# Optimization experiments

Hardware: AMD Instinct MI355X
Metric: run time of the kernel (lower is better)

Reference implementation:

```python
import jax, jax.numpy as jnp
import numpy as np

B, CIN, H, W = 128, 64, 32, 32
COUT, K, STRIDE, PAD = 64, 3, 1, 1
HO = (H + 2 * PAD - K) // STRIDE + 1
WO = (W + 2 * PAD - K) // STRIDE + 1


def setup_inputs() -> dict:
    key = jax.random.key(0)
    k1, k2 = jax.random.split(key)
    x = jax.random.normal(k1, (B, CIN, H, W), dtype=jnp.float32)
    # weight scaled like torch init: randn / sqrt(k*k*Cin) (orthogonal_ in torch just
    # re-orthogonalizes; scale here matches the fan-in normalization)
    weight = jax.random.normal(k2, (HO, WO, COUT, CIN, K, K), dtype=jnp.float32) / np.sqrt(K * K * CIN)
    bias = jnp.full((COUT, HO, WO), 0.5, dtype=jnp.float32)
    return {"x": x, "weight": weight, "bias": bias}


def reference(x, weight, bias):
    # pad spatial dims
    xp = jnp.pad(x, ((0, 0), (0, 0), (PAD, PAD), (PAD, PAD)))
    # gather row windows: [B, C, Ho, K, Wp]
    ri = (jnp.arange(HO) * STRIDE)[:, None] + jnp.arange(K)[None, :]  # [Ho, K]
    ci = (jnp.arange(WO) * STRIDE)[:, None] + jnp.arange(K)[None, :]  # [Wo, K]
    rows = xp[:, :, ri, :]           # [B, C, Ho, K, Wp]
    patches = rows[:, :, :, :, ci]   # [B, C, Ho, K, Wo, K]
    # per-location matmul: b c h p w q , h w d c p q -> b d h w
    out = jnp.einsum('bchpwq,hwdcpq->bdhw', patches, weight)
    return out + bias[None]
```

## Files before the change

### kernel.cpp

```cpp
#include <hip/hip_runtime.h>
#include <hip/hip_bf16.h>

#define KT 576

typedef __attribute__((ext_vector_type(8))) short  short8;
typedef __attribute__((ext_vector_type(4))) float  f32x4;

__device__ __forceinline__ unsigned short f2bf(float f) {
  union { float f; unsigned int u; } v; v.f = f;
  return (unsigned short)((v.u + 0x7FFFu + ((v.u >> 16) & 1u)) >> 16);
}

__global__ __launch_bounds__(256) void xC2_kernel(const float* __restrict__ x,
                                                  unsigned short* __restrict__ xC2) {
  const int hp = blockIdx.x, bb = blockIdx.y, t = threadIdx.x;
  __shared__ unsigned short tile[32 * 1024];
  const bool interior = (hp >= 1 && hp <= 32);
  if (interior) {
#pragma unroll 4
    for (int i = 0; i < 32; ++i) {
      const int row = i * 32 + (t >> 3);
      const int bl = row >> 6, c = row & 63;
      const int k = t & 7;
      const float4 v = *(const float4*)(x + ((size_t)(bb * 16 + bl) * 64 + c) * 1024 +
                                        (hp - 1) * 32 + k * 4);
      const int base = (k * 4) * 1024 + (c >> 3) * 128 + bl * 8 + (c & 7);
      tile[base]        = f2bf(v.x);
      tile[base + 1024] = f2bf(v.y);
      tile[base + 2048] = f2bf(v.z);
      tile[base + 3072] = f2bf(v.w);
    }
  }
  __syncthreads();
  unsigned short* dst = xC2 + (size_t)hp * 278528 + (size_t)bb * 1024;
  const uint4 z = make_uint4(0u, 0u, 0u, 0u);
  for (int idx = t; idx < 34 * 128; idx += 256) {
    const int wp = idx >> 7, s = idx & 127;
    uint4 v = z;
    if (interior && wp >= 1 && wp <= 32) v = *(const uint4*)&tile[(wp - 1) * 1024 + s * 8];
    *(uint4*)(dst + (size_t)wp * 8192 + s * 8) = v;
  }
}

__global__ __launch_bounds__(256, 4) void lc_main(const float* __restrict__ Wt,
                                                  const float* __restrict__ bias,
                                                  const unsigned short* __restrict__ xC2,
                                                  float* __restrict__ out,
                                                  float* __restrict__ tmp,
                                                  int useTmp) {
  __shared__ unsigned short Wl[32 * KT];
  __shared__ float blds[32];

  const int bid = (int)blockIdx.x;
  const int swz = (bid & 7) * 256 + (bid >> 3);
  const int hw = swz >> 1, half = swz & 1;
  const int h = hw >> 5, w = hw & 31;
  const int t = threadIdx.x, lane = t & 63, wv = t >> 6;
  const int l15 = lane & 15, lg = lane >> 4;

  if (t < 32) blds[t] = bias[(half * 32 + t) * 1024 + hw];

  const float* Wsrc = Wt + (size_t)hw * (64 * KT) + (size_t)half * (32 * KT);
  float4 wreg[18];
#pragma unroll
  for (int i = 0; i < 18; ++i)
    wreg[i] = ((const float4*)Wsrc)[i * 256 + t];
#pragma unroll
  for (int i = 0; i < 18; ++i) {
    const int f = (i * 256 + t) * 4;
    const int d = (((unsigned)(f >> 6)) * 7282u) >> 16;
    int kn = f - d * 576;
    int c = ((unsigned)kn * 7282u) >> 16;
    int r = kn - c * 9;
    const float vv[4] = {wreg[i].x, wreg[i].y, wreg[i].z, wreg[i].w};
#pragma unroll
    for (int j = 0; j < 4; ++j) {
      const int kp = r * 64 + c;
      const int slot = (kp >> 3) ^ (d & 7);
      Wl[d * KT + slot * 8 + (kp & 7)] = f2bf(vv[j]);
      if (++r == 9) { r = 0; ++c; }
    }
  }
  __syncthreads();

  const unsigned short* xA = xC2 + (size_t)wv * 2048 + lg * 128 + l15 * 8;

  f32x4 acc[2][2];
#pragma unroll
  for (int bt = 0; bt < 2; ++bt)
#pragma unroll
    for (int dt = 0; dt < 2; ++dt) acc[bt][dt] = (f32x4){0.f, 0.f, 0.f, 0.f};

  const int x7 = l15 & 7;
  const int wrow0 = l15 * KT;
  const int wrow1 = (16 + l15) * KT;

  short8 A0[2][3], A1[2][3];
#pragma unroll
  for (int s = 0; s < 3; ++s) {
    const int pq = s >> 1, p = pq / 3, q = pq - p * 3;
    const size_t off = (size_t)(h + p) * 278528 + (size_t)(w + q) * 8192 + (s & 1) * 512;
    A0[0][s] = *(const short8*)(xA + off);
    A1[0][s] = *(const short8*)(xA + off + 1024);
  }
#pragma unroll
  for (int g = 0; g < 6; ++g) {
    const int cur = g & 1;
    if (g < 5) {
#pragma unroll
      for (int s = 0; s < 3; ++s) {
        const int step = (g + 1) * 3 + s;
        const int pq = step >> 1, p = pq / 3, q = pq - p * 3;
        const size_t off = (size_t)(h + p) * 278528 + (size_t)(w + q) * 8192 + (step & 1) * 512;
        A0[cur ^ 1][s] = *(const short8*)(xA + off);
        A1[cur ^ 1][s] = *(const short8*)(xA + off + 1024);
      }
    }
#pragma unroll
    for (int s = 0; s < 3; ++s) {
      const int step = g * 3 + s;
      const int sb = step * 4 + lg;
      const short8 b0 = *(const short8*)&Wl[wrow0 + ((sb ^ x7) << 3)];
      const short8 b1 = *(const short8*)&Wl[wrow1 + ((sb ^ x7) << 3)];
      acc[0][0] = __builtin_amdgcn_mfma_f32_16x16x32_bf16(A0[cur][s], b0, acc[0][0], 0, 0, 0);
      acc[1][0] = __builtin_amdgcn_mfma_f32_16x16x32_bf16(A1[cur][s], b0, acc[1][0], 0, 0, 0);
      acc[0][1] = __builtin_amdgcn_mfma_f32_16x16x32_bf16(A0[cur][s], b1, acc[0][1], 0, 0, 0);
      acc[1][1] = __builtin_amdgcn_mfma_f32_16x16x32_bf16(A1[cur][s], b1, acc[1][1], 0, 0, 0);
    }
  }

  if (useTmp) {
    float* tb = tmp + (size_t)(hw * 2 + half) * (32 * 128) + wv * 32;
#pragma unroll
    for (int dt = 0; dt < 2; ++dt) {
      const float bv = blds[dt * 16 + l15];
#pragma unroll
      for (int bt = 0; bt < 2; ++bt) {
        f32x4 v = acc[bt][dt];
        v[0] += bv; v[1] += bv; v[2] += bv; v[3] += bv;
        *(f32x4*)(tb + (dt * 16 + l15) * 128 + bt * 16 + lg * 4) = v;
      }
    }
  } else {
#pragma unroll
    for (int dt = 0; dt < 2; ++dt) {
      const int dg = half * 32 + dt * 16 + l15;
      const float bv = blds[dt * 16 + l15];
#pragma unroll
      for (int bt = 0; bt < 2; ++bt) {
#pragma unroll
        for (int i = 0; i < 4; ++i) {
          const int b = wv * 32 + bt * 16 + lg * 4 + i;
          out[(size_t)b * 65536 + (size_t)dg * 1024 + hw] = acc[bt][dt][i] + bv;
        }
      }
    }
  }
}

__global__ __launch_bounds__(256) void tr_out(const float* __restrict__ tmp,
                                              float* __restrict__ out) {
  const int h = blockIdx.x;
  const int d = blockIdx.y;
  const int half = d >> 5, dl = d & 31;
  const int t = threadIdx.x;
  __shared__ float ls[32 * 132];
  {
    const int w = t >> 3, bc = t & 7;
    const float* src = tmp + ((size_t)((h * 32 + w) * 2 + half) * 32 + dl) * 128 + bc * 16;
    float* dst = ls + w * 132 + bc * 16;
#pragma unroll
    for (int k = 0; k < 4; ++k) ((float4*)dst)[k] = ((const float4*)src)[k];
  }
  __syncthreads();
  {
    const int b = t >> 1, wh = t & 1;
    float4 o[4];
#pragma unroll
    for (int k = 0; k < 4; ++k)
#pragma unroll
      for (int j = 0; j < 4; ++j)
        ((float*)&o[k])[j] = ls[(wh * 16 + k * 4 + j) * 132 + b];
    float* dst = out + (size_t)b * 65536 + (size_t)d * 1024 + h * 32 + wh * 16;
#pragma unroll
    for (int k = 0; k < 4; ++k) ((float4*)dst)[k] = o[k];
  }
}

extern "C" void kernel_launch(void* const* d_in, const int* in_sizes, int n_in,
                              void* d_out, int out_size, void* d_ws, size_t ws_size,
                              hipStream_t stream) {
  const float* x    = (const float*)d_in[0];
  const float* wt   = (const float*)d_in[1];
  const float* bias = (const float*)d_in[2];
  float* out        = (float*)d_out;

  unsigned short* xC2 = (unsigned short*)d_ws;
  const size_t XC2_BYTES = 18939904u;
  const size_t TMP_BYTES = 33554432u;
  const int useTmp = (ws_size >= XC2_BYTES + TMP_BYTES) ? 1 : 0;
  float* tmp = (float*)((char*)d_ws + XC2_BYTES);

  xC2_kernel<<<dim3(34, 8), 256, 0, stream>>>(x, xC2);
  lc_main<<<2048, 256, 0, stream>>>(wt, bias, xC2, out, tmp, useTmp);
  if (useTmp) tr_out<<<dim3(32, 64), 256, 0, stream>>>(tmp, out);
}
```

Baseline: 72.85 us.

## Drop transposed temp buffer pass and write output directly; split weight loads into batches

Removes the intermediate tmp buffer and the separate transpose kernel, so the main kernel always scatters results straight to the output with strided 4-byte stores. The weight staging is split into two batches of nine float4 loads with a scheduling barrier, which lowers register pressure. The change saves a 32MB round trip through memory and one launch, but the direct stores are uncoalesced, one element per 4KB stride.

After: 83.05 us. 14.0% more time.

```diff
diff --git a/kernel.cpp b/kernel.cpp
--- a/kernel.cpp
+++ b/kernel.cpp
@@ -45,9 +45,7 @@
 __global__ __launch_bounds__(256, 4) void lc_main(const float* __restrict__ Wt,
                                                   const float* __restrict__ bias,
                                                   const unsigned short* __restrict__ xC2,
-                                                  float* __restrict__ out,
-                                                  float* __restrict__ tmp,
-                                                  int useTmp) {
+                                                  float* __restrict__ out) {
   __shared__ unsigned short Wl[32 * KT];
   __shared__ float blds[32];
 
@@ -61,24 +59,28 @@
   if (t < 32) blds[t] = bias[(half * 32 + t) * 1024 + hw];
 
   const float* Wsrc = Wt + (size_t)hw * (64 * KT) + (size_t)half * (32 * KT);
-  float4 wreg[18];
 #pragma unroll
-  for (int i = 0; i < 18; ++i)
-    wreg[i] = ((const float4*)Wsrc)[i * 256 + t];
+  for (int bat = 0; bat < 2; ++bat) {
+    float4 wreg[9];
 #pragma unroll
-  for (int i = 0; i < 18; ++i) {
-    const int f = (i * 256 + t) * 4;
-    const int d = (((unsigned)(f >> 6)) * 7282u) >> 16;
-    int kn = f - d * 576;
-    int c = ((unsigned)kn * 7282u) >> 16;
-    int r = kn - c * 9;
-    const float vv[4] = {wreg[i].x, wreg[i].y, wreg[i].z, wreg[i].w};
+    for (int i = 0; i < 9; ++i)
+      wreg[i] = ((const float4*)Wsrc)[(bat * 9 + i) * 256 + t];
+    __builtin_amdgcn_sched_barrier(0);
 #pragma unroll
-    for (int j = 0; j < 4; ++j) {
-      const int kp = r * 64 + c;
-      const int slot = (kp >> 3) ^ (d & 7);
-      Wl[d * KT + slot * 8 + (kp & 7)] = f2bf(vv[j]);
-      if (++r == 9) { r = 0; ++c; }
+    for (int i = 0; i < 9; ++i) {
+      const int f = ((bat * 9 + i) * 256 + t) * 4;
+      const int d = (((unsigned)(f >> 6)) * 7282u) >> 16;
+      int kn = f - d * 576;
+      int c = ((unsigned)kn * 7282u) >> 16;
+      int r = kn - c * 9;
+      const float vv[4] = {wreg[i].x, wreg[i].y, wreg[i].z, wreg[i].w};
+#pragma unroll
+      for (int j = 0; j < 4; ++j) {
+        const int kp = r * 64 + c;
+        const int slot = (kp >> 3) ^ (d & 7);
+        Wl[d * KT + slot * 8 + (kp & 7)] = f2bf(vv[j]);
+        if (++r == 9) { r = 0; ++c; }
+      }
     }
   }
   __syncthreads();
@@ -129,61 +131,18 @@
     }
   }
 
-  if (useTmp) {
-    float* tb = tmp + (size_t)(hw * 2 + half) * (32 * 128) + wv * 32;
 #pragma unroll
-    for (int dt = 0; dt < 2; ++dt) {
-      const float bv = blds[dt * 16 + l15];
+  for (int dt = 0; dt < 2; ++dt) {
+    const int dg = half * 32 + dt * 16 + l15;
+    const float bv = blds[dt * 16 + l15];
 #pragma unroll
-      for (int bt = 0; bt < 2; ++bt) {
-        f32x4 v = acc[bt][dt];
-        v[0] += bv; v[1] += bv; v[2] += bv; v[3] += bv;
-        *(f32x4*)(tb + (dt * 16 + l15) * 128 + bt * 16 + lg * 4) = v;
+    for (int bt = 0; bt < 2; ++bt) {
+#pragma unroll
+      for (int i = 0; i < 4; ++i) {
+        const int b = wv * 32 + bt * 16 + lg * 4 + i;
+        out[(size_t)b * 65536 + (size_t)dg * 1024 + hw] = acc[bt][dt][i] + bv;
       }
     }
-  } else {
-#pragma unroll
-    for (int dt = 0; dt < 2; ++dt) {
-      const int dg = half * 32 + dt * 16 + l15;
-      const float bv = blds[dt * 16 + l15];
-#pragma unroll
-      for (int bt = 0; bt < 2; ++bt) {
-#pragma unroll
-        for (int i = 0; i < 4; ++i) {
-          const int b = wv * 32 + bt * 16 + lg * 4 + i;
-          out[(size_t)b * 65536 + (size_t)dg * 1024 + hw] = acc[bt][dt][i] + bv;
-        }
-      }
-    }
-  }
-}
-
-__global__ __launch_bounds__(256) void tr_out(const float* __restrict__ tmp,
-                                              float* __restrict__ out) {
-  const int h = blockIdx.x;
-  const int d = blockIdx.y;
-  const int half = d >> 5, dl = d & 31;
-  const int t = threadIdx.x;
-  __shared__ float ls[32 * 132];
-  {
-    const int w = t >> 3, bc = t & 7;
-    const float* src = tmp + ((size_t)((h * 32 + w) * 2 + half) * 32 + dl) * 128 + bc * 16;
-    float* dst = ls + w * 132 + bc * 16;
-#pragma unroll
-    for (int k = 0; k < 4; ++k) ((float4*)dst)[k] = ((const float4*)src)[k];
-  }
-  __syncthreads();
-  {
-    const int b = t >> 1, wh = t & 1;
-    float4 o[4];
-#pragma unroll
-    for (int k = 0; k < 4; ++k)
-#pragma unroll
-      for (int j = 0; j < 4; ++j)
-        ((float*)&o[k])[j] = ls[(wh * 16 + k * 4 + j) * 132 + b];
-    float* dst = out + (size_t)b * 65536 + (size_t)d * 1024 + h * 32 + wh * 16;
-#pragma unroll
-    for (int k = 0; k < 4; ++k) ((float4*)dst)[k] = o[k];
   }
 }
 
@@ -194,14 +153,8 @@
   const float* wt   = (const float*)d_in[1];
   const float* bias = (const float*)d_in[2];
   float* out        = (float*)d_out;
-
   unsigned short* xC2 = (unsigned short*)d_ws;
-  const size_t XC2_BYTES = 18939904u;
-  const size_t TMP_BYTES = 33554432u;
-  const int useTmp = (ws_size >= XC2_BYTES + TMP_BYTES) ? 1 : 0;
-  float* tmp = (float*)((char*)d_ws + XC2_BYTES);
 
   xC2_kernel<<<dim3(34, 8), 256, 0, stream>>>(x, xC2);
-  lc_main<<<2048, 256, 0, stream>>>(wt, bias, xC2, out, tmp, useTmp);
-  if (useTmp) tr_out<<<dim3(32, 64), 256, 0, stream>>>(tmp, out);
+  lc_main<<<2048, 256, 0, stream>>>(wt, bias, xC2, out);
 }
```

## Split weight staging in two batches and hand-schedule global loads with waitcnt

Applied to the files above, without the earlier changes.

The weight load-and-convert into LDS is split into two batches of nine float4 loads, which roughly halves the peak register footprint. The first activation tiles are issued alongside the second batch. All global loads are now inline asm with explicit s_waitcnt vmcnt counts and sched_barriers, so the prefetch of the next A tiles overlaps the MFMAs of the current group. The goal is lower register pressure and controlled latency hiding. The risk is that manual waitcnt accounting conflicts with compiler-generated loads, and that the barriers block useful scheduling.

Result: no change. 72.56 us (-0.4%).

```diff
diff --git a/kernel.cpp b/kernel.cpp
--- a/kernel.cpp
+++ b/kernel.cpp
@@ -61,48 +61,59 @@
   if (t < 32) blds[t] = bias[(half * 32 + t) * 1024 + hw];
 
   const float* Wsrc = Wt + (size_t)hw * (64 * KT) + (size_t)half * (32 * KT);
-  float4 wreg[18];
-#pragma unroll
-  for (int i = 0; i < 18; ++i)
-    wreg[i] = ((const float4*)Wsrc)[i * 256 + t];
-#pragma unroll
-  for (int i = 0; i < 18; ++i) {
-    const int f = (i * 256 + t) * 4;
-    const int d = (((unsigned)(f >> 6)) * 7282u) >> 16;
-    int kn = f - d * 576;
-    int c = ((unsigned)kn * 7282u) >> 16;
-    int r = kn - c * 9;
-    const float vv[4] = {wreg[i].x, wreg[i].y, wreg[i].z, wreg[i].w};
-#pragma unroll
-    for (int j = 0; j < 4; ++j) {
-      const int kp = r * 64 + c;
-      const int slot = (kp >> 3) ^ (d & 7);
-      Wl[d * KT + slot * 8 + (kp & 7)] = f2bf(vv[j]);
-      if (++r == 9) { r = 0; ++c; }
+  const unsigned short* xA = xC2 + (size_t)wv * 2048 + lg * 128 + l15 * 8;
+
+  short8 A0[2][3], A1[2][3];
+  f32x4 acc[2][2];
+#pragma unroll
+  for (int bt = 0; bt < 2; ++bt)
+#pragma unroll
+    for (int dt = 0; dt < 2; ++dt) acc[bt][dt] = (f32x4){0.f, 0.f, 0.f, 0.f};
+
+#pragma unroll
+  for (int bat = 0; bat < 2; ++bat) {
+    float4 wreg[9];
+#pragma unroll
+    for (int i = 0; i < 9; ++i) {
+      const float4* p = (const float4*)Wsrc + ((bat * 9 + i) * 256 + t);
+      asm volatile("global_load_dwordx4 %0, %1, off" : "=v"(wreg[i]) : "v"(p));
+    }
+    if (bat == 1) {
+#pragma unroll
+      for (int s = 0; s < 3; ++s) {
+        const int pq = s >> 1, p = pq / 3, q = pq - p * 3;
+        const size_t off = (size_t)(h + p) * 278528 + (size_t)(w + q) * 8192 + (s & 1) * 512;
+        const short8* p0 = (const short8*)(xA + off);
+        const short8* p1 = (const short8*)(xA + off + 1024);
+        asm volatile("global_load_dwordx4 %0, %1, off" : "=v"(A0[0][s]) : "v"(p0));
+        asm volatile("global_load_dwordx4 %0, %1, off" : "=v"(A1[0][s]) : "v"(p1));
+      }
+    }
+    asm volatile("s_waitcnt vmcnt(0)" ::: "memory");
+    __builtin_amdgcn_sched_barrier(0);
+#pragma unroll
+    for (int i = 0; i < 9; ++i) {
+      const int f = ((bat * 9 + i) * 256 + t) * 4;
+      const int d = (((unsigned)(f >> 6)) * 7282u) >> 16;
+      int kn = f - d * 576;
+      int c = ((unsigned)kn * 7282u) >> 16;
+      int r = kn - c * 9;
+      const float vv[4] = {wreg[i].x, wreg[i].y, wreg[i].z, wreg[i].w};
+#pragma unroll
+      for (int j = 0; j < 4; ++j) {
+        const int kp = r * 64 + c;
+        const int slot = (kp >> 3) ^ (d & 7);
+        Wl[d * KT + slot * 8 + (kp & 7)] = f2bf(vv[j]);
+        if (++r == 9) { r = 0; ++c; }
+      }
     }
   }
   __syncthreads();
-
-  const unsigned short* xA = xC2 + (size_t)wv * 2048 + lg * 128 + l15 * 8;
-
-  f32x4 acc[2][2];
-#pragma unroll
-  for (int bt = 0; bt < 2; ++bt)
-#pragma unroll
-    for (int dt = 0; dt < 2; ++dt) acc[bt][dt] = (f32x4){0.f, 0.f, 0.f, 0.f};
 
   const int x7 = l15 & 7;
   const int wrow0 = l15 * KT;
   const int wrow1 = (16 + l15) * KT;
 
-  short8 A0[2][3], A1[2][3];
-#pragma unroll
-  for (int s = 0; s < 3; ++s) {
-    const int pq = s >> 1, p = pq / 3, q = pq - p * 3;
-    const size_t off = (size_t)(h + p) * 278528 + (size_t)(w + q) * 8192 + (s & 1) * 512;
-    A0[0][s] = *(const short8*)(xA + off);
-    A1[0][s] = *(const short8*)(xA + off + 1024);
-  }
 #pragma unroll
   for (int g = 0; g < 6; ++g) {
     const int cur = g & 1;
@@ -112,10 +123,16 @@
         const int step = (g + 1) * 3 + s;
         const int pq = step >> 1, p = pq / 3, q = pq - p * 3;
         const size_t off = (size_t)(h + p) * 278528 + (size_t)(w + q) * 8192 + (step & 1) * 512;
-        A0[cur ^ 1][s] = *(const short8*)(xA + off);
-        A1[cur ^ 1][s] = *(const short8*)(xA + off + 1024);
-      }
-    }
+        const short8* p0 = (const short8*)(xA + off);
+        const short8* p1 = (const short8*)(xA + off + 1024);
+        asm volatile("global_load_dwordx4 %0, %1, off" : "=v"(A0[cur ^ 1][s]) : "v"(p0));
+        asm volatile("global_load_dwordx4 %0, %1, off" : "=v"(A1[cur ^ 1][s]) : "v"(p1));
+      }
+      asm volatile("s_waitcnt vmcnt(6)" ::: "memory");
+    } else {
+      asm volatile("s_waitcnt vmcnt(0)" ::: "memory");
+    }
+    __builtin_amdgcn_sched_barrier(0);
 #pragma unroll
     for (int s = 0; s < 3; ++s) {
       const int step = g * 3 + s;
```
